# Kernel optimization log

Measured on AMD Instinct MI355X. Metric: run time of the kernel, lower is better.

## Reference

```python
import jax, jax.numpy as jnp
import numpy as np

N, E, D, ED, FD, H, Q, K, G = 50000, 600000, 128, 128, 512, 1, 3, 512, 512
NEG_SLOPE = 0.2
EPS = 1e-5


def setup_inputs() -> dict:
    key = jax.random.key(0)
    ks = jax.random.split(key, 16)
    inp = {
        'x': jax.random.normal(ks[0], (N, D), jnp.float32),
        'edge_index': jax.random.randint(ks[1], (2, E), 0, N, jnp.int32),
        'edge_attr': jax.random.normal(ks[2], (E, ED), jnp.float32),
        'batch_vec': jnp.sort(jax.random.randint(ks[3], (N,), 0, G, jnp.int32)),
        'W_l': jax.random.normal(ks[4], (D, H * D), jnp.float32),
        'b_l': jnp.zeros((H * D,), jnp.float32),
        'W_r': jax.random.normal(ks[5], (D, H * D), jnp.float32),
        'b_r': jnp.zeros((H * D,), jnp.float32),
        'W_edge': jax.random.normal(ks[6], (ED, H * D), jnp.float32),
        'att': jax.random.normal(ks[7], (H, D), jnp.float32),
        'conv_bias': jnp.zeros((H * D,), jnp.float32),
        'adapter_W': jax.random.normal(ks[8], (D, D), jnp.float32),
        'adapter_b': jnp.zeros((D,), jnp.float32),
        'norm_g': jnp.ones((D,), jnp.float32),
        'norm_b': jnp.zeros((D,), jnp.float32),
        'codebooks': jax.random.normal(ks[9], (Q, K, D), jnp.float32),
        'out_W': jax.random.normal(ks[10], (D, FD), jnp.float32),
        'out_b': jnp.zeros((FD,), jnp.float32),
        'outnorm_g': jnp.ones((FD,), jnp.float32),
        'outnorm_b': jnp.zeros((FD,), jnp.float32),
    }
    return inp


def _layer_norm(x, g, b):
    m = x.mean(-1, keepdims=True)
    v = ((x - m) ** 2).mean(-1, keepdims=True)
    return (x - m) * jax.lax.rsqrt(v + EPS) * g + b


def _forward(x, edge_index, edge_attr, batch_vec, W_l, b_l, W_r, b_r, W_edge, att,
             conv_bias, adapter_W, adapter_b, norm_g, norm_b, codebooks, out_W, out_b,
             outnorm_g, outnorm_b):
    sg = jax.lax.stop_gradient
    n = x.shape[0]
    # ---- GATv2Conv (PyG defaults: add_self_loops=True, fill_value='mean') ----
    loops = jnp.arange(n, dtype=edge_index.dtype)
    src = jnp.concatenate([edge_index[0], loops])
    dst = jnp.concatenate([edge_index[1], loops])
    mean_attr = edge_attr.mean(0)
    ea = jnp.concatenate([edge_attr, jnp.broadcast_to(mean_attr, (n, edge_attr.shape[1]))])
    xl = (x @ W_l + b_l).reshape(n, H, D)   # source transform
    xr = (x @ W_r + b_r).reshape(n, H, D)   # target transform
    e_emb = (ea @ W_edge).reshape(-1, H, D)
    e = xl[src] + xr[dst] + e_emb           # [Etot,H,D]
    score = jnp.einsum('ehd,hd->eh', jax.nn.leaky_relu(e, NEG_SLOPE), att)
    smax = jax.ops.segment_max(score, dst, num_segments=n)
    ex = jnp.exp(score - smax[dst])
    denom = jax.ops.segment_sum(ex, dst, num_segments=n)
    alpha = ex / (denom[dst] + 1e-16)       # per-target softmax
    out = jax.ops.segment_sum(xl[src] * alpha[..., None], dst, num_segments=n)  # [n,H,D]
    out = out.reshape(n, H * D) + conv_bias
    h = out.reshape(n, H, D).mean(1)        # mean over heads
    # ---- global mean pool over graphs ----
    sums = jax.ops.segment_sum(h, batch_vec, num_segments=G)
    cnts = jax.ops.segment_sum(jnp.ones((n,), h.dtype), batch_vec, num_segments=G)
    g = sums / jnp.maximum(cnts, 1.0)[:, None]
    # ---- adapter + layernorm ----
    g = g @ adapter_W + adapter_b
    g = _layer_norm(g, norm_g, norm_b)
    # ---- residual VQ (euclidean nearest code, straight-through) ----
    residual = g
    quantized_out = jnp.zeros_like(g)
    codes, idxs, commits = [], [], []
    cb_sq = (codebooks ** 2).sum(-1)        # [Q,K]
    for q in range(Q):
        cb = codebooks[q]
        d2 = (residual ** 2).sum(-1, keepdims=True) - 2.0 * residual @ cb.T + cb_sq[q]
        idx = jnp.argmin(d2, axis=-1)
        code = cb[idx]
        commits.append(((sg(code) - residual) ** 2).mean())
        quantized_out = quantized_out + residual + sg(code - residual)
        codes.append(code)
        idxs.append(idx)
        residual = residual - sg(code)
    commit_loss = jnp.stack(commits).mean()
    residual_loss = ((g - quantized_out) ** 2).mean()
    loss = commit_loss + residual_loss
    indices = jnp.stack(idxs, axis=1)       # [G,Q]
    # ---- per-quantizer straight-through tokens -> projection -> layernorm ----
    tokens = jnp.stack([g + sg(c - g) for c in codes], axis=1)  # [G,Q,D]
    tokens = tokens @ out_W + out_b                              # [G,Q,FD]
    tokens = _layer_norm(tokens, outnorm_g, outnorm_b)
    return tokens, indices, loss


def reference(x, edge_index, edge_attr, batch_vec, W_l, b_l, W_r, b_r, W_edge, att,
              conv_bias, adapter_W, adapter_b, norm_g, norm_b, codebooks, out_W, out_b,
              outnorm_g, outnorm_b):
    return _forward(x, edge_index, edge_attr, batch_vec, W_l, b_l, W_r, b_r, W_edge,
                    att, conv_bias, adapter_W, adapter_b, norm_g, norm_b, codebooks,
                    out_W, out_b, outnorm_g, outnorm_b)
```

## Files before the change

kernel.cpp:

```cpp
#include <hip/hip_runtime.h>
#include <math.h>

#define N_NODES 50000
#define E_EDGES 600000
#define DD 128
#define G_GRAPHS 512
#define K_CODES 512
#define Q_QUANT 3
#define FD_OUT 512
#define NEG_SLOPE 0.2f
#define LN_EPS 1e-5f

static __device__ __forceinline__ float lrelu(float v){ return v > 0.f ? v : NEG_SLOPE*v; }
static __device__ __forceinline__ float wsum(float v){
#pragma unroll
  for (int m = 1; m < 64; m <<= 1) v += __shfl_xor(v, m);
  return v;
}
static __device__ __forceinline__ float wmax(float v){
#pragma unroll
  for (int m = 1; m < 64; m <<= 1) v = fmaxf(v, __shfl_xor(v, m));
  return v;
}

#define EA_LD 130

__global__ __launch_bounds__(256)
void k_xform2(const float* __restrict__ x,
              const float* __restrict__ W_l, const float* __restrict__ b_l,
              const float* __restrict__ W_r, const float* __restrict__ b_r,
              float* __restrict__ xl, float* __restrict__ xr, int n)
{
  __shared__ __align__(16) float xt[64*EA_LD];
  __shared__ __align__(16) float WtL[32*128];
  __shared__ __align__(16) float WtR[32*128];
  const int tid = threadIdx.x;
  const int r0 = blockIdx.x * 64;
  {
    const int q = tid & 63, eb = tid >> 6;
#pragma unroll
    for (int i = 0; i < 16; ++i){
      int e = eb + 4*i;
      int row = r0 + e;
      float2 v = make_float2(0.f, 0.f);
      if (row < n) v = *(const float2*)&x[row*DD + q*2];
      *(float2*)&xt[e*EA_LD + q*2] = v;
    }
  }
  const int eg = tid >> 4;
  const int cg = tid & 15;
  float accL[4][8], accR[4][8];
#pragma unroll
  for (int j = 0; j < 4; ++j)
#pragma unroll
    for (int u = 0; u < 8; ++u){ accL[j][u] = 0.f; accR[j][u] = 0.f; }

  for (int kq = 0; kq < 4; ++kq){
    __syncthreads();
    {
      const int c4 = tid & 31, kb = tid >> 5;
#pragma unroll
      for (int i = 0; i < 4; ++i){
        int kk = kb + 8*i;
        *(float4*)&WtL[kk*128 + c4*4] = *(const float4*)&W_l[(kq*32+kk)*DD + c4*4];
        *(float4*)&WtR[kk*128 + c4*4] = *(const float4*)&W_r[(kq*32+kk)*DD + c4*4];
      }
    }
    __syncthreads();
    const int kb2 = kq*32;
#pragma unroll 4
    for (int k = 0; k < 32; ++k){
      float aa[4];
#pragma unroll
      for (int j = 0; j < 4; ++j) aa[j] = xt[(eg*4+j)*EA_LD + kb2 + k];
      float bL[8], bR[8];
      *(float4*)&bL[0] = *(const float4*)&WtL[k*128 + cg*4];
      *(float4*)&bL[4] = *(const float4*)&WtL[k*128 + 64 + cg*4];
      *(float4*)&bR[0] = *(const float4*)&WtR[k*128 + cg*4];
      *(float4*)&bR[4] = *(const float4*)&WtR[k*128 + 64 + cg*4];
#pragma unroll
      for (int j = 0; j < 4; ++j){
#pragma unroll
        for (int u = 0; u < 8; ++u) accL[j][u] = fmaf(aa[j], bL[u], accL[j][u]);
#pragma unroll
        for (int u = 0; u < 8; ++u) accR[j][u] = fmaf(aa[j], bR[u], accR[j][u]);
      }
    }
  }
  float bvL[8], bvR[8];
  *(float4*)&bvL[0] = *(const float4*)&b_l[cg*4];
  *(float4*)&bvL[4] = *(const float4*)&b_l[64 + cg*4];
  *(float4*)&bvR[0] = *(const float4*)&b_r[cg*4];
  *(float4*)&bvR[4] = *(const float4*)&b_r[64 + cg*4];
#pragma unroll
  for (int j = 0; j < 4; ++j){
    int row = r0 + eg*4 + j;
    if (row < n){
      float oL[8], oR[8];
#pragma unroll
      for (int u = 0; u < 8; ++u){ oL[u] = accL[j][u] + bvL[u]; oR[u] = accR[j][u] + bvR[u]; }
      *(float4*)&xl[row*DD + cg*4]      = *(const float4*)&oL[0];
      *(float4*)&xl[row*DD + 64 + cg*4] = *(const float4*)&oL[4];
      *(float4*)&xr[row*DD + cg*4]      = *(const float4*)&oR[0];
      *(float4*)&xr[row*DD + 64 + cg*4] = *(const float4*)&oR[4];
    }
  }
}

__global__ __launch_bounds__(256)
void k_edge(const float* __restrict__ edge_attr, const float* __restrict__ W_edge,
            const int* __restrict__ ei, const float* __restrict__ xl,
            const float* __restrict__ xr, const float* __restrict__ att,
            const int* __restrict__ off, int* __restrict__ pos,
            uint2* __restrict__ rec, float* __restrict__ asum_mid)
{
  __shared__ __align__(16) float ea[64*EA_LD];
  __shared__ __align__(16) float Wt[32*128];
  const int tid = threadIdx.x;
  const int e0 = blockIdx.x * 64;
  const int eg = tid >> 4;
  const int cg = tid & 15;
  int dsts[4], srcs[4];
#pragma unroll
  for (int j = 0; j < 4; ++j){
    int e = e0 + eg*4 + j;
    srcs[j] = ei[e];
    dsts[j] = ei[E_EDGES + e];
  }
  {
    const int q = tid & 63, eb = tid >> 6;
#pragma unroll
    for (int i = 0; i < 16; ++i){
      int e = eb + 4*i;
      *(float2*)&ea[e*EA_LD + q*2] = *(const float2*)&edge_attr[(e0+e)*DD + q*2];
    }
  }
  float acc[4][8];
#pragma unroll
  for (int j = 0; j < 4; ++j)
#pragma unroll
    for (int u = 0; u < 8; ++u) acc[j][u] = 0.f;

  for (int kq = 0; kq < 4; ++kq){
    __syncthreads();
    {
      const int c4 = tid & 31, kb = tid >> 5;
#pragma unroll
      for (int i = 0; i < 4; ++i){
        int kk = kb + 8*i;
        *(float4*)&Wt[kk*128 + c4*4] = *(const float4*)&W_edge[(kq*32+kk)*DD + c4*4];
      }
    }
    __syncthreads();
    const int kb2 = kq*32;
#pragma unroll 4
    for (int k = 0; k < 32; ++k){
      float aa[4];
#pragma unroll
      for (int j = 0; j < 4; ++j) aa[j] = ea[(eg*4+j)*EA_LD + kb2 + k];
      float bb[8];
      *(float4*)&bb[0] = *(const float4*)&Wt[k*128 + cg*4];
      *(float4*)&bb[4] = *(const float4*)&Wt[k*128 + 64 + cg*4];
#pragma unroll
      for (int j = 0; j < 4; ++j)
#pragma unroll
        for (int u = 0; u < 8; ++u) acc[j][u] = fmaf(aa[j], bb[u], acc[j][u]);
    }
  }
  float attv[8];
  *(float4*)&attv[0] = *(const float4*)&att[cg*4];
  *(float4*)&attv[4] = *(const float4*)&att[64 + cg*4];
  float sp[4];
#pragma unroll
  for (int j = 0; j < 4; ++j){
    float xlv[8], xrv[8];
    *(float4*)&xlv[0] = *(const float4*)&xl[srcs[j]*DD + cg*4];
    *(float4*)&xlv[4] = *(const float4*)&xl[srcs[j]*DD + 64 + cg*4];
    *(float4*)&xrv[0] = *(const float4*)&xr[dsts[j]*DD + cg*4];
    *(float4*)&xrv[4] = *(const float4*)&xr[dsts[j]*DD + 64 + cg*4];
    float p = 0.f;
#pragma unroll
    for (int u = 0; u < 8; ++u){
      float vv = acc[j][u] + xlv[u] + xrv[u];
      p += lrelu(vv) * attv[u];
    }
    sp[j] = p;
  }
#pragma unroll
  for (int m = 1; m < 16; m <<= 1){
#pragma unroll
    for (int j = 0; j < 4; ++j) sp[j] += __shfl_xor(sp[j], m);
  }
  if (cg == 0){
#pragma unroll
    for (int j = 0; j < 4; ++j){
      int d = dsts[j];
      int p = atomicAdd(&pos[d], 1);
      uint2 r;
      r.x = (unsigned)srcs[j];
      r.y = __float_as_uint(sp[j]);
      rec[off[d] + p] = r;
    }
  }
  if (tid < 128){
    float s = 0.f;
    for (int e = 0; e < 64; ++e) s += ea[e*EA_LD + tid];
    atomicAdd(&asum_mid[(blockIdx.x & 63)*DD + tid], s);
  }
}

__global__ __launch_bounds__(128)
void k_me(const float* __restrict__ asum_mid, const float* __restrict__ W_edge,
          float* __restrict__ me)
{
  __shared__ float mean[128];
  const int d = threadIdx.x;
  float s = 0.f;
  for (int r = 0; r < 64; ++r) s += asum_mid[r*DD + d];
  mean[d] = s / (float)E_EDGES;
  __syncthreads();
  float acc = 0.f;
  for (int k = 0; k < 128; ++k) acc += mean[k] * W_edge[k*DD + d];
  me[d] = acc;
}

__global__ __launch_bounds__(256)
void k_hist(const int* __restrict__ ei, int* __restrict__ indeg)
{
  int e = blockIdx.x*256 + threadIdx.x;
  if (e < E_EDGES) atomicAdd(&indeg[ei[E_EDGES + e]], 1);
}

__global__ __launch_bounds__(256)
void k_cbsq(const float* __restrict__ codebooks, double* __restrict__ cbsqd)
{
  const int tid = threadIdx.x;
  const int cl = tid >> 2, dq = tid & 3;
  const int code = blockIdx.x*64 + cl;
  const float4* cp = (const float4*)&codebooks[(size_t)code*DD + dq*32];
  double cc = 0.0;
#pragma unroll
  for (int i = 0; i < 8; ++i){
    float4 cv = cp[i];
    cc += (double)cv.x*cv.x + (double)cv.y*cv.y + (double)cv.z*cv.z + (double)cv.w*cv.w;
  }
  cc += __shfl_xor(cc, 1); cc += __shfl_xor(cc, 2);
  if (dq == 0) cbsqd[code] = cc;
}

#define SC_NB ((N_NODES + 511) / 512)
__global__ __launch_bounds__(512)
void k_scan1(const int* __restrict__ indeg, int* __restrict__ off, int* __restrict__ bsum)
{
  __shared__ int s[512];
  const int tid = threadIdx.x;
  const int gid = blockIdx.x*512 + tid;
  int v = (gid < N_NODES) ? indeg[gid] : 0;
  s[tid] = v;
  __syncthreads();
  for (int d = 1; d < 512; d <<= 1){
    int t = (tid >= d) ? s[tid-d] : 0;
    __syncthreads();
    s[tid] += t;
    __syncthreads();
  }
  if (gid < N_NODES) off[gid] = s[tid] - v;
  if (tid == 511) bsum[blockIdx.x] = s[511];
}

__global__ __launch_bounds__(128)
void k_scan2(const int* __restrict__ bsum, int* __restrict__ boff)
{
  __shared__ int s[128];
  const int tid = threadIdx.x;
  int v = (tid < SC_NB) ? bsum[tid] : 0;
  s[tid] = v;
  __syncthreads();
  for (int d = 1; d < 128; d <<= 1){
    int t = (tid >= d) ? s[tid-d] : 0;
    __syncthreads();
    s[tid] += t;
    __syncthreads();
  }
  if (tid < SC_NB) boff[tid] = s[tid] - v;
}

__global__ __launch_bounds__(512)
void k_scan3(int* __restrict__ off, const int* __restrict__ boff)
{
  const int gid = blockIdx.x*512 + threadIdx.x;
  if (gid < N_NODES) off[gid] += boff[blockIdx.x];
  if (gid == 0) off[N_NODES] = E_EDGES;
}

__global__ __launch_bounds__(256)
void k_aggregate(const int* __restrict__ off, const uint2* __restrict__ rec,
                 const float* __restrict__ xl, const float* __restrict__ xr,
                 const float* __restrict__ me, const float* __restrict__ att,
                 const float* __restrict__ conv_bias, const int* __restrict__ batch_vec,
                 float* __restrict__ gsum, float* __restrict__ gcnt)
{
  __shared__ float hshare[4][128];
  __shared__ int bsh[4];
  const int tid = threadIdx.x, lane = tid & 63, wid = tid >> 6;
  const int i = blockIdx.x*4 + wid;
  float2 xli = *(const float2*)&xl[i*DD + lane*2];
  float2 xri = *(const float2*)&xr[i*DD + lane*2];
  float2 mev = *(const float2*)&me[lane*2];
  float2 attv = *(const float2*)&att[lane*2];
  float v0 = xli.x + xri.x + mev.x;
  float v1 = xli.y + xri.y + mev.y;
  float s_self = wsum(lrelu(v0)*attv.x + lrelu(v1)*attv.y);
  const int o0 = off[i], o1 = off[i+1];
  const int deg = o1 - o0;
  uint2 myrec = make_uint2(0u, __float_as_uint(-INFINITY));
  float m = s_self;
  if (lane < deg) myrec = rec[o0 + lane];
  m = fmaxf(m, __uint_as_float(myrec.y));
  for (int b = 64; b < deg; b += 64){
    int j = b + lane;
    if (j < deg) m = fmaxf(m, __uint_as_float(rec[o0 + j].y));
  }
  m = wmax(m);
  float wse = __expf(s_self - m);
  float den = wse;
  float a0 = wse * xli.x, a1 = wse * xli.y;
  if (deg <= 64){
    float msc = __uint_as_float(myrec.y);
    int msrc = (int)myrec.x;
#pragma unroll 4
    for (int j = 0; j < deg; ++j){
      float sc = __shfl(msc, j);
      int s = __shfl(msrc, j);
      float w = __expf(sc - m);
      den += w;
      float2 xs = *(const float2*)&xl[s*DD + lane*2];
      a0 = fmaf(w, xs.x, a0);
      a1 = fmaf(w, xs.y, a1);
    }
  } else {
#pragma unroll 4
    for (int j = 0; j < deg; ++j){
      uint2 r = rec[o0 + j];
      float w = __expf(__uint_as_float(r.y) - m);
      den += w;
      float2 xs = *(const float2*)&xl[(int)r.x*DD + lane*2];
      a0 = fmaf(w, xs.x, a0);
      a1 = fmaf(w, xs.y, a1);
    }
  }
  float inv = 1.0f / (den + 1e-16f);
  float2 cb2 = *(const float2*)&conv_bias[lane*2];
  float h0 = a0*inv + cb2.x;
  float h1 = a1*inv + cb2.y;
  int b = batch_vec[i];
  hshare[wid][lane*2]     = h0;
  hshare[wid][lane*2 + 1] = h1;
  if (lane == 0) bsh[wid] = b;
  __syncthreads();
  bool uni = (bsh[0]==bsh[1]) && (bsh[1]==bsh[2]) && (bsh[2]==bsh[3]);
  if (uni){
    if (wid == 0){
      float s0 = hshare[0][lane*2] + hshare[1][lane*2] + hshare[2][lane*2] + hshare[3][lane*2];
      float s1 = hshare[0][lane*2+1] + hshare[1][lane*2+1] + hshare[2][lane*2+1] + hshare[3][lane*2+1];
      atomicAdd(&gsum[b*DD + lane*2],     s0);
      atomicAdd(&gsum[b*DD + lane*2 + 1], s1);
      if (lane == 0) atomicAdd(&gcnt[b], 4.0f);
    }
  } else {
    atomicAdd(&gsum[b*DD + lane*2],     h0);
    atomicAdd(&gsum[b*DD + lane*2 + 1], h1);
    if (lane == 0) atomicAdd(&gcnt[b], 1.0f);
  }
}

__global__ __launch_bounds__(256)
void k_rvq(const float* __restrict__ gsum, const float* __restrict__ gcnt,
           const float* __restrict__ aW, const float* __restrict__ ab,
           const float* __restrict__ ng, const float* __restrict__ nb,
           const double* __restrict__ cbsqd, const float* __restrict__ codebooks,
           float* __restrict__ ind_out, int* __restrict__ idx_i,
           float* __restrict__ accs)
{
  __shared__ __align__(16) float r_lds[128];
  __shared__ float red[128];
  __shared__ float row[128];
  __shared__ double bd[64];
  __shared__ int bi[64];
  __shared__ int chosen;
  const int g = blockIdx.x, tid = threadIdx.x;

  if (tid < 128){
    float denom = fmaxf(gcnt[g], 1.0f);
    row[tid] = gsum[g*DD + tid] / denom;
  }
  __syncthreads();
  float aval = 0.f;
  if (tid < 128){
    double accd = (double)ab[tid];
    for (int k = 0; k < 128; ++k) accd += (double)row[k] * (double)aW[k*DD + tid];
    aval = (float)accd;
    red[tid] = aval;
  }
  __syncthreads();
  for (int s = 64; s > 0; s >>= 1){ if (tid < s) red[tid] += red[tid+s]; __syncthreads(); }
  float mean = red[0] / 128.f; __syncthreads();
  float cdev = aval - mean;
  if (tid < 128) red[tid] = cdev*cdev;
  __syncthreads();
  for (int s = 64; s > 0; s >>= 1){ if (tid < s) red[tid] += red[tid+s]; __syncthreads(); }
  float var = red[0] / 128.f; __syncthreads();
  float linv = (float)(1.0 / sqrt((double)var + (double)LN_EPS));
  if (tid < 128) r_lds[tid] = cdev * linv * ng[tid] + nb[tid];
  __syncthreads();

  const int cl = tid >> 2, dq = tid & 3;
  for (int q = 0; q < Q_QUANT; ++q){
    const float* cb = codebooks + (size_t)q * K_CODES * DD;
    const double* cbs = cbsqd + (size_t)q * K_CODES;
    double bestd = 1e300; int besti = 1 << 30;
    for (int r = 0; r < 8; ++r){
      int c = r*64 + cl;
      double rc = 0.0;
      const float4* cp = (const float4*)&cb[c*DD + dq*32];
      const float4* rp = (const float4*)&r_lds[dq*32];
#pragma unroll
      for (int i = 0; i < 8; ++i){
        float4 cv = cp[i]; float4 rv = rp[i];
        rc += (double)cv.x*rv.x + (double)cv.y*rv.y + (double)cv.z*rv.z + (double)cv.w*rv.w;
      }
      rc += __shfl_xor(rc, 1); rc += __shfl_xor(rc, 2);
      if (dq == 0){
        double d2 = cbs[c] - 2.0*rc;
        if (d2 < bestd || (d2 == bestd && c < besti)){ bestd = d2; besti = c; }
      }
    }
    if (dq == 0){ bd[cl] = bestd; bi[cl] = besti; }
    __syncthreads();
    if (tid < 64){
      double d2 = bd[tid]; int ii = bi[tid];
#pragma unroll
      for (int m = 1; m < 64; m <<= 1){
        double od = __shfl_xor(d2, m); int oi = __shfl_xor(ii, m);
        if (od < d2 || (od == d2 && oi < ii)){ d2 = od; ii = oi; }
      }
      if (tid == 0) chosen = ii;
    }
    __syncthreads();
    const int idx = chosen;
    if (tid == 0){
      ind_out[g*Q_QUANT + q] = (float)idx;
      idx_i[g*Q_QUANT + q] = idx;
    }
    if (tid < 128){
      float cd = cb[idx*DD + tid];
      float diff = cd - r_lds[tid];
      red[tid] = diff * diff;
      r_lds[tid] -= cd;
    }
    __syncthreads();
    for (int s = 64; s > 0; s >>= 1){ if (tid < s) red[tid] += red[tid+s]; __syncthreads(); }
    if (tid == 0) atomicAdd(&accs[q], red[0]);
    __syncthreads();
  }
  if (tid < 128) red[tid] = r_lds[tid]*r_lds[tid];
  __syncthreads();
  for (int s = 64; s > 0; s >>= 1){ if (tid < s) red[tid] += red[tid+s]; __syncthreads(); }
  if (tid == 0) atomicAdd(&accs[3], red[0]);
}

__global__ __launch_bounds__(256)
void k_tokens(const float* __restrict__ codebooks, const int* __restrict__ idx_i,
              const float* __restrict__ out_W, const float* __restrict__ out_b,
              const float* __restrict__ og, const float* __restrict__ ob,
              const float* __restrict__ accs,
              float* __restrict__ tokens, float* __restrict__ loss_out)
{
  __shared__ __align__(16) float c_lds[128];
  __shared__ float red[256];
  const int blk = blockIdx.x;
  const int g = blk / 3, q = blk % 3;
  const int tid = threadIdx.x;
  if (blk == 0 && tid == 0){
    float commit = (accs[0] + accs[1] + accs[2]) / (3.0f * G_GRAPHS * DD);
    float resid  = accs[3] / ((float)G_GRAPHS * DD);
    loss_out[0] = commit + resid;
  }
  const int idx = idx_i[g*Q_QUANT + q];
  if (tid < 128) c_lds[tid] = codebooks[((size_t)q*K_CODES + idx)*DD + tid];
  __syncthreads();
  double v0 = (double)out_b[tid];
  double v1 = (double)out_b[tid + 256];
  for (int k = 0; k < 128; ++k){
    double ck = (double)c_lds[k];
    v0 += ck * (double)out_W[k*FD_OUT + tid];
    v1 += ck * (double)out_W[k*FD_OUT + tid + 256];
  }
  float f0 = (float)v0, f1 = (float)v1;
  red[tid] = f0 + f1; __syncthreads();
  for (int s = 128; s > 0; s >>= 1){ if (tid < s) red[tid] += red[tid+s]; __syncthreads(); }
  float mean = red[0] / 512.f; __syncthreads();
  float d0 = f0 - mean, d1 = f1 - mean;
  red[tid] = d0*d0 + d1*d1; __syncthreads();
  for (int s = 128; s > 0; s >>= 1){ if (tid < s) red[tid] += red[tid+s]; __syncthreads(); }
  float var = red[0] / 512.f; __syncthreads();
  float inv = (float)(1.0 / sqrt((double)var + (double)LN_EPS));
  tokens[(size_t)blk*FD_OUT + tid]       = d0*inv*og[tid] + ob[tid];
  tokens[(size_t)blk*FD_OUT + tid + 256] = d1*inv*og[tid+256] + ob[tid+256];
}

extern "C" void kernel_launch(void* const* d_in, const int* in_sizes, int n_in,
                              void* d_out, int out_size, void* d_ws, size_t ws_size,
                              hipStream_t stream)
{
  (void)in_sizes; (void)n_in; (void)out_size; (void)ws_size;
  const float* x         = (const float*)d_in[0];
  const int*   ei        = (const int*)d_in[1];
  const float* edge_attr = (const float*)d_in[2];
  const int*   batch_vec = (const int*)d_in[3];
  const float* W_l       = (const float*)d_in[4];
  const float* b_l       = (const float*)d_in[5];
  const float* W_r       = (const float*)d_in[6];
  const float* b_r       = (const float*)d_in[7];
  const float* W_edge    = (const float*)d_in[8];
  const float* att       = (const float*)d_in[9];
  const float* conv_bias = (const float*)d_in[10];
  const float* aW        = (const float*)d_in[11];
  const float* ab        = (const float*)d_in[12];
  const float* ng        = (const float*)d_in[13];
  const float* nb        = (const float*)d_in[14];
  const float* codebooks = (const float*)d_in[15];
  const float* out_W     = (const float*)d_in[16];
  const float* out_b     = (const float*)d_in[17];
  const float* og        = (const float*)d_in[18];
  const float* ob        = (const float*)d_in[19];
  float* outf = (float*)d_out;

  char* w = (char*)d_ws;
  size_t o = 0;
  auto nxt = [&](size_t bytes)->void*{
    void* p = w + o;
    o += (bytes + 511) & ~(size_t)511;
    return p;
  };
  int*   indeg    = (int*)  nxt((size_t)N_NODES*4);
  int*   pos      = (int*)  nxt((size_t)N_NODES*4);
  float* asum_mid = (float*)nxt((size_t)64*DD*4);
  float* gsum     = (float*)nxt((size_t)G_GRAPHS*DD*4);
  float* gcnt     = (float*)nxt((size_t)G_GRAPHS*4);
  float* accs     = (float*)nxt(16);
  const size_t zero_span = o;
  int*   off      = (int*)  nxt((size_t)(N_NODES+1)*4);
  float* xl       = (float*)nxt((size_t)N_NODES*DD*4);
  float* xr       = (float*)nxt((size_t)N_NODES*DD*4);
  uint2* rec      = (uint2*)nxt((size_t)E_EDGES*8);
  float* me       = (float*)nxt((size_t)DD*4);
  int*   idx_i    = (int*)  nxt((size_t)G_GRAPHS*Q_QUANT*4);
  int*   bsum     = (int*)  nxt((size_t)SC_NB*4);
  int*   boff     = (int*)  nxt((size_t)SC_NB*4);
  double* cbsqd   = (double*)nxt((size_t)Q_QUANT*K_CODES*8);

  hipMemsetAsync(w, 0, zero_span, stream);

  k_cbsq<<<dim3(Q_QUANT*K_CODES/64), dim3(256), 0, stream>>>(codebooks, cbsqd);
  k_hist<<<dim3((E_EDGES+255)/256), dim3(256), 0, stream>>>(ei, indeg);
  k_scan1<<<dim3(SC_NB), dim3(512), 0, stream>>>(indeg, off, bsum);
  k_scan2<<<dim3(1), dim3(128), 0, stream>>>(bsum, boff);
  k_scan3<<<dim3(SC_NB), dim3(512), 0, stream>>>(off, boff);
  k_xform2<<<dim3((N_NODES+63)/64), dim3(256), 0, stream>>>(x, W_l, b_l, W_r, b_r,
                                                            xl, xr, N_NODES);
  k_edge<<<dim3(E_EDGES/64), dim3(256), 0, stream>>>(edge_attr, W_edge, ei, xl, xr, att,
                                                     off, pos, rec, asum_mid);
  k_me<<<dim3(1), dim3(128), 0, stream>>>(asum_mid, W_edge, me);
  k_aggregate<<<dim3(N_NODES/4), dim3(256), 0, stream>>>(off, rec, xl, xr, me, att,
                                                         conv_bias, batch_vec, gsum, gcnt);
  k_rvq<<<dim3(G_GRAPHS), dim3(256), 0, stream>>>(gsum, gcnt, aW, ab, ng, nb, cbsqd,
                                                  codebooks,
                                                  outf + (size_t)G_GRAPHS*Q_QUANT*FD_OUT,
                                                  idx_i, accs);
  k_tokens<<<dim3(G_GRAPHS*Q_QUANT), dim3(256), 0, stream>>>(codebooks, idx_i, out_W, out_b,
                                                             og, ob, accs, outf,
                                                             outf + (size_t)G_GRAPHS*Q_QUANT*FD_OUT
                                                                  + (size_t)G_GRAPHS*Q_QUANT);
}
```

Measured before the change: 586.6 us.

## Process four nodes per wavefront in GAT aggregation with 16-lane groups

The aggregation kernel now gives each destination node a 16-lane group instead of a full 64-lane wave, so one wave handles four nodes. Each lane loads 8 contiguous features with float4 loads, and the reductions and neighbor shuffles stay inside the group. Each block now covers 16 nodes, which widens the per-graph atomic pre-reduction and cuts the number of global atomics. The aim is more memory-level parallelism on the neighbor gathers and less shuffle and atomic overhead. The cost is divergence when nodes in one wave have different degrees, and only nodes with degree up to 16 take the shuffle fast path.

```diff
diff --git a/kernel.cpp b/kernel.cpp
--- a/kernel.cpp
+++ b/kernel.cpp
@@ -12,14 +12,14 @@
 #define LN_EPS 1e-5f
 
 static __device__ __forceinline__ float lrelu(float v){ return v > 0.f ? v : NEG_SLOPE*v; }
-static __device__ __forceinline__ float wsum(float v){
-#pragma unroll
-  for (int m = 1; m < 64; m <<= 1) v += __shfl_xor(v, m);
+static __device__ __forceinline__ float wsum16(float v){
+#pragma unroll
+  for (int m = 1; m < 16; m <<= 1) v += __shfl_xor(v, m);
   return v;
 }
-static __device__ __forceinline__ float wmax(float v){
-#pragma unroll
-  for (int m = 1; m < 64; m <<= 1) v = fmaxf(v, __shfl_xor(v, m));
+static __device__ __forceinline__ float wmax16(float v){
+#pragma unroll
+  for (int m = 1; m < 16; m <<= 1) v = fmaxf(v, __shfl_xor(v, m));
   return v;
 }
 
@@ -300,77 +300,98 @@
                  const float* __restrict__ conv_bias, const int* __restrict__ batch_vec,
                  float* __restrict__ gsum, float* __restrict__ gcnt)
 {
-  __shared__ float hshare[4][128];
-  __shared__ int bsh[4];
-  const int tid = threadIdx.x, lane = tid & 63, wid = tid >> 6;
-  const int i = blockIdx.x*4 + wid;
-  float2 xli = *(const float2*)&xl[i*DD + lane*2];
-  float2 xri = *(const float2*)&xr[i*DD + lane*2];
-  float2 mev = *(const float2*)&me[lane*2];
-  float2 attv = *(const float2*)&att[lane*2];
-  float v0 = xli.x + xri.x + mev.x;
-  float v1 = xli.y + xri.y + mev.y;
-  float s_self = wsum(lrelu(v0)*attv.x + lrelu(v1)*attv.y);
+  __shared__ float hshare[16][128];
+  __shared__ int bsh[16];
+  const int tid = threadIdx.x, lane = tid & 63, w = tid >> 6;
+  const int q4 = lane >> 4, l16 = lane & 15;
+  const int node_slot = w*4 + q4;
+  const int i = blockIdx.x*16 + node_slot;
+  const int sbase = lane & 48;
+
+  float xli[8], xri[8], mev[8], attv[8];
+  *(float4*)&xli[0] = *(const float4*)&xl[(size_t)i*DD + l16*8];
+  *(float4*)&xli[4] = *(const float4*)&xl[(size_t)i*DD + l16*8 + 4];
+  *(float4*)&xri[0] = *(const float4*)&xr[(size_t)i*DD + l16*8];
+  *(float4*)&xri[4] = *(const float4*)&xr[(size_t)i*DD + l16*8 + 4];
+  *(float4*)&mev[0] = *(const float4*)&me[l16*8];
+  *(float4*)&mev[4] = *(const float4*)&me[l16*8 + 4];
+  *(float4*)&attv[0] = *(const float4*)&att[l16*8];
+  *(float4*)&attv[4] = *(const float4*)&att[l16*8 + 4];
+  float p = 0.f;
+#pragma unroll
+  for (int u = 0; u < 8; ++u) p += lrelu(xli[u] + xri[u] + mev[u]) * attv[u];
+  float s_self = wsum16(p);
   const int o0 = off[i], o1 = off[i+1];
   const int deg = o1 - o0;
   uint2 myrec = make_uint2(0u, __float_as_uint(-INFINITY));
   float m = s_self;
-  if (lane < deg) myrec = rec[o0 + lane];
+  if (l16 < deg) myrec = rec[o0 + l16];
   m = fmaxf(m, __uint_as_float(myrec.y));
-  for (int b = 64; b < deg; b += 64){
-    int j = b + lane;
+  for (int b = 16; b < deg; b += 16){
+    int j = b + l16;
     if (j < deg) m = fmaxf(m, __uint_as_float(rec[o0 + j].y));
   }
-  m = wmax(m);
+  m = wmax16(m);
   float wse = __expf(s_self - m);
   float den = wse;
-  float a0 = wse * xli.x, a1 = wse * xli.y;
-  if (deg <= 64){
+  float a[8];
+#pragma unroll
+  for (int u = 0; u < 8; ++u) a[u] = wse * xli[u];
+  if (deg <= 16){
     float msc = __uint_as_float(myrec.y);
     int msrc = (int)myrec.x;
 #pragma unroll 4
     for (int j = 0; j < deg; ++j){
-      float sc = __shfl(msc, j);
-      int s = __shfl(msrc, j);
-      float w = __expf(sc - m);
-      den += w;
-      float2 xs = *(const float2*)&xl[s*DD + lane*2];
-      a0 = fmaf(w, xs.x, a0);
-      a1 = fmaf(w, xs.y, a1);
+      float sc = __shfl(msc, sbase + j);
+      int s = __shfl(msrc, sbase + j);
+      float w_ = __expf(sc - m);
+      den += w_;
+      float xs[8];
+      *(float4*)&xs[0] = *(const float4*)&xl[(size_t)s*DD + l16*8];
+      *(float4*)&xs[4] = *(const float4*)&xl[(size_t)s*DD + l16*8 + 4];
+#pragma unroll
+      for (int u = 0; u < 8; ++u) a[u] = fmaf(w_, xs[u], a[u]);
     }
   } else {
 #pragma unroll 4
     for (int j = 0; j < deg; ++j){
       uint2 r = rec[o0 + j];
-      float w = __expf(__uint_as_float(r.y) - m);
-      den += w;
-      float2 xs = *(const float2*)&xl[(int)r.x*DD + lane*2];
-      a0 = fmaf(w, xs.x, a0);
-      a1 = fmaf(w, xs.y, a1);
+      float w_ = __expf(__uint_as_float(r.y) - m);
+      den += w_;
+      float xs[8];
+      *(float4*)&xs[0] = *(const float4*)&xl[(size_t)(int)r.x*DD + l16*8];
+      *(float4*)&xs[4] = *(const float4*)&xl[(size_t)(int)r.x*DD + l16*8 + 4];
+#pragma unroll
+      for (int u = 0; u < 8; ++u) a[u] = fmaf(w_, xs[u], a[u]);
     }
   }
   float inv = 1.0f / (den + 1e-16f);
-  float2 cb2 = *(const float2*)&conv_bias[lane*2];
-  float h0 = a0*inv + cb2.x;
-  float h1 = a1*inv + cb2.y;
-  int b = batch_vec[i];
-  hshare[wid][lane*2]     = h0;
-  hshare[wid][lane*2 + 1] = h1;
-  if (lane == 0) bsh[wid] = b;
-  __syncthreads();
-  bool uni = (bsh[0]==bsh[1]) && (bsh[1]==bsh[2]) && (bsh[2]==bsh[3]);
+  float cb8[8], hv[8];
+  *(float4*)&cb8[0] = *(const float4*)&conv_bias[l16*8];
+  *(float4*)&cb8[4] = *(const float4*)&conv_bias[l16*8 + 4];
+#pragma unroll
+  for (int u = 0; u < 8; ++u) hv[u] = a[u]*inv + cb8[u];
+  const int b = batch_vec[i];
+  *(float4*)&hshare[node_slot][l16*8]     = *(const float4*)&hv[0];
+  *(float4*)&hshare[node_slot][l16*8 + 4] = *(const float4*)&hv[4];
+  if (l16 == 0) bsh[node_slot] = b;
+  __syncthreads();
+  bool uni = true;
+#pragma unroll
+  for (int k = 1; k < 16; ++k) uni = uni && (bsh[k] == bsh[0]);
   if (uni){
-    if (wid == 0){
-      float s0 = hshare[0][lane*2] + hshare[1][lane*2] + hshare[2][lane*2] + hshare[3][lane*2];
-      float s1 = hshare[0][lane*2+1] + hshare[1][lane*2+1] + hshare[2][lane*2+1] + hshare[3][lane*2+1];
-      atomicAdd(&gsum[b*DD + lane*2],     s0);
-      atomicAdd(&gsum[b*DD + lane*2 + 1], s1);
-      if (lane == 0) atomicAdd(&gcnt[b], 4.0f);
-    }
+    if (tid < 128){
+      float s = 0.f;
+#pragma unroll
+      for (int k = 0; k < 16; ++k) s += hshare[k][tid];
+      atomicAdd(&gsum[bsh[0]*DD + tid], s);
+    }
+    if (tid == 0) atomicAdd(&gcnt[bsh[0]], 16.0f);
   } else {
-    atomicAdd(&gsum[b*DD + lane*2],     h0);
-    atomicAdd(&gsum[b*DD + lane*2 + 1], h1);
-    if (lane == 0) atomicAdd(&gcnt[b], 1.0f);
+#pragma unroll
+    for (int u = 0; u < 8; ++u)
+      atomicAdd(&gsum[b*DD + l16*8 + u], hv[u]);
+    if (l16 == 0) atomicAdd(&gcnt[b], 1.0f);
   }
 }
 
@@ -572,8 +593,8 @@
   k_edge<<<dim3(E_EDGES/64), dim3(256), 0, stream>>>(edge_attr, W_edge, ei, xl, xr, att,
                                                      off, pos, rec, asum_mid);
   k_me<<<dim3(1), dim3(128), 0, stream>>>(asum_mid, W_edge, me);
-  k_aggregate<<<dim3(N_NODES/4), dim3(256), 0, stream>>>(off, rec, xl, xr, me, att,
-                                                         conv_bias, batch_vec, gsum, gcnt);
+  k_aggregate<<<dim3(N_NODES/16), dim3(256), 0, stream>>>(off, rec, xl, xr, me, att,
+                                                          conv_bias, batch_vec, gsum, gcnt);
   k_rvq<<<dim3(G_GRAPHS), dim3(256), 0, stream>>>(gsum, gcnt, aW, ab, ng, nb, cbsqd,
                                                   codebooks,
                                                   outf + (size_t)G_GRAPHS*Q_QUANT*FD_OUT,
```

New measurement: 600.7 us. 2.4% more time.
